# Kernel optimization log

Measured on AMD Instinct MI355X. Metric: run time of the kernel, lower is better.

The kernel has to match this reference:

```python
import jax, jax.numpy as jnp
import numpy as np

BETA = 0.25
B, D, H, W = 32, 256, 32, 32
K = 1024


def setup_inputs() -> dict:
    key = jax.random.key(0)
    k1, k2 = jax.random.split(key)
    inputs = jax.random.normal(k1, (B, D, H, W), dtype=jnp.float32)
    # torch init: uniform(-1/K, 1/K)
    codebook = jax.random.uniform(k2, (K, D), dtype=jnp.float32,
                                  minval=-1.0 / K, maxval=1.0 / K)
    return {"inputs": inputs, "codebook": codebook}


def reference(inputs, codebook):
    b, d, h, w = inputs.shape
    # (B, C, H, W) -> (B*H*W, D)
    x = inputs.transpose(0, 2, 3, 1).reshape(b * h * w, d)
    # Squared Euclidean distances; argmin is identical to cdist argmin.
    x2 = jnp.sum(x * x, axis=1, keepdims=True)            # (N, 1)
    c2 = jnp.sum(codebook * codebook, axis=1)             # (K,)
    d2 = x2 - 2.0 * (x @ codebook.T) + c2[None, :]        # (N, K)
    idx = jnp.argmin(d2, axis=1)                          # (N,)
    q = codebook[idx].reshape(b, h, w, d).transpose(0, 3, 1, 2)  # (B, D, H, W)

    q_loss = jnp.mean((q - jax.lax.stop_gradient(inputs)) ** 2)
    e_loss = jnp.mean((jax.lax.stop_gradient(q) - inputs) ** 2)
    vq_loss = q_loss + BETA * e_loss

    # straight-through estimator
    quantized = inputs + jax.lax.stop_gradient(q - inputs)
    return quantized, q_loss, e_loss, vq_loss, idx.reshape(b, h, w)
```

## Files before the change

kernel.cpp:

```cpp
#include <hip/hip_runtime.h>
#include <cstdint>

typedef float floatx4 __attribute__((ext_vector_type(4)));
typedef _Float16 half8 __attribute__((ext_vector_type(8)));
typedef _Float16 half4v __attribute__((ext_vector_type(4)));

#define D_DIM 256
#define HW 1024
#define K_CODES 1024
#define NPIX 32768
#define NELEM 8388608

#define OFF_QLOSS 8388608
#define OFF_ELOSS 8388609
#define OFF_VQ    8388610
#define OFF_IDX   8388611

#define WS_IDX     0
#define WS_C2      131072
#define WS_CNT     135168
#define WS_PART    135232
#define WS_FLAGPX  143424
#define WS_FLAGTOP 176192
#define WS_CBS     438336
#define FLAG_CAP   8192

#define MARGIN 2.5e-4f

__device__ __forceinline__ float np_pairwise_sq_256(const float* __restrict__ a, int stride) {
    float half[2];
#pragma unroll
    for (int h = 0; h < 2; ++h) {
        const float* p = a + (size_t)(h * 128) * stride;
        float r[8];
#pragma unroll
        for (int j = 0; j < 8; ++j) { float t = p[(size_t)j * stride]; r[j] = __fmul_rn(t, t); }
        for (int i = 8; i < 128; i += 8)
#pragma unroll
            for (int j = 0; j < 8; ++j) {
                float t = p[(size_t)(i + j) * stride];
                r[j] = __fadd_rn(r[j], __fmul_rn(t, t));
            }
        half[h] = __fadd_rn(__fadd_rn(__fadd_rn(r[0], r[1]), __fadd_rn(r[2], r[3])),
                            __fadd_rn(__fadd_rn(r[4], r[5]), __fadd_rn(r[6], r[7])));
    }
    return __fadd_rn(half[0], half[1]);
}

__global__ __launch_bounds__(256) void prep_kernel(const float* __restrict__ cb,
                                                   _Float16* __restrict__ cbs,
                                                   float* __restrict__ c2,
                                                   int* __restrict__ cnt) {
    int b = blockIdx.x;
    if (b < 256) {
        int idx = b * 256 + threadIdx.x;
        int c = idx >> 6;
        int d = (idx & 63) * 4;
        int s = d >> 5, q = (d >> 3) & 3, j0 = d & 7;
        int half = c >> 9, ch = (c >> 4) & 31, l15 = c & 15;
        int lane = q * 16 + l15;
        size_t o = ((((size_t)(half * 32 + ch) * 8 + s) * 64 + lane) * 8 + j0);
        floatx4 v = *(const floatx4*)(cb + (size_t)c * D_DIM + d);
        half4v h;
#pragma unroll
        for (int j = 0; j < 4; ++j) h[j] = (_Float16)(v[j] * 1024.0f);
        *(half4v*)(cbs + o) = h;
    } else {
        if (b == 256 && threadIdx.x == 0) *cnt = 0;
        int k = (b - 256) * 256 + threadIdx.x;
        c2[k] = np_pairwise_sq_256(cb + (size_t)k * D_DIM, 1);
    }
}

__device__ __forceinline__ void ins4v(float v, int k, float* S, int* I) {
    if (v < S[3]) {
        S[3] = v; I[3] = k;
#pragma unroll
        for (int j = 3; j > 0; --j) {
            if (S[j] < S[j - 1]) {
                float ts = S[j]; S[j] = S[j - 1]; S[j - 1] = ts;
                int   ti = I[j]; I[j] = I[j - 1]; I[j - 1] = ti;
            }
        }
    }
}

__global__ __launch_bounds__(256, 2) void gemm_swz(
        const float* __restrict__ x, const _Float16* __restrict__ cbs,
        const float* __restrict__ c2, float* __restrict__ out_idx,
        int* __restrict__ idxbuf, int* __restrict__ cnt,
        int* __restrict__ flagPx, floatx4* __restrict__ flagTop) {
    __shared__ float scr[4][32 * 33];

    const int t = threadIdx.x;
    const int w = t >> 6;
    const int l = t & 63;
    const int l15 = l & 15;
    const int q = l >> 4;
    const int pxg = w >> 1;
    const int half = w & 1;
    const int px0 = blockIdx.x * 32;
    const int bimg = px0 >> 10;
    const int hwb = (px0 & 1023) + pxg * 16;
    const float* xb = x + (size_t)bimg * (D_DIM * HW);

    half8 A[8];
    {
        float tmp[64];
#pragma unroll
        for (int s = 0; s < 8; ++s)
#pragma unroll
            for (int j = 0; j < 8; ++j)
                tmp[s * 8 + j] = xb[(size_t)(s * 32 + q * 8 + j) * HW + hwb + l15];
#pragma unroll
        for (int s = 0; s < 8; ++s) {
            half8 h;
#pragma unroll
            for (int j = 0; j < 8; ++j) h[j] = (_Float16)tmp[s * 8 + j];
            A[s] = h;
        }
    }

    const _Float16* base = cbs + (size_t)half * 131072;
    half8 B[2][8];
#pragma unroll
    for (int s = 0; s < 8; ++s)
        B[0][s] = *(const half8*)(base + (size_t)s * 512 + l * 8);
    float c2cur = c2[half * 512 + l15];

    float m1[4], m2[4]; int i1[4], i2[4];
#pragma unroll
    for (int a = 0; a < 4; ++a) {
        m1[a] = INFINITY; m2[a] = INFINITY; i1[a] = 0; i2[a] = 0;
    }

#pragma unroll 4
    for (int ch = 0; ch < 32; ++ch) {
        const int cur = ch & 1, nxt = cur ^ 1;
        float c2n = 0.f;
        if (ch < 31) {
            const _Float16* nb = base + (size_t)(ch + 1) * 4096;
#pragma unroll
            for (int s = 0; s < 8; ++s)
                B[nxt][s] = *(const half8*)(nb + (size_t)s * 512 + l * 8);
            c2n = c2[half * 512 + (ch + 1) * 16 + l15];
        }
        floatx4 ac[2];
        ac[0] = floatx4{0.f, 0.f, 0.f, 0.f};
        ac[1] = floatx4{0.f, 0.f, 0.f, 0.f};
#pragma unroll
        for (int s = 0; s < 4; ++s) {
            ac[0] = __builtin_amdgcn_mfma_f32_16x16x32_f16(A[s],     B[cur][s],     ac[0], 0, 0, 0);
            ac[1] = __builtin_amdgcn_mfma_f32_16x16x32_f16(A[s + 4], B[cur][s + 4], ac[1], 0, 0, 0);
        }
        const int code = half * 512 + ch * 16 + l15;
#pragma unroll
        for (int a = 0; a < 4; ++a) {
            float dot = ac[0][a] + ac[1][a];
            float s = fmaf(-0.001953125f, dot, c2cur);
            if (s < m1[a]) { m2[a] = m1[a]; i2[a] = i1[a]; m1[a] = s; i1[a] = code; }
            else if (s < m2[a]) { m2[a] = s; i2[a] = code; }
        }
        c2cur = c2n;
    }

    const int part = half * 16 + l15;
#pragma unroll
    for (int a = 0; a < 4; ++a) {
        int px = pxg * 16 + q * 4 + a;
        int o = part * 33 + px;
        scr[0][o] = m1[a];
        scr[1][o] = __int_as_float(i1[a]);
        scr[2][o] = m2[a];
        scr[3][o] = __int_as_float(i2[a]);
    }
    __syncthreads();
    if (t < 32) {
        float S[4] = {INFINITY, INFINITY, INFINITY, INFINITY};
        int   I[4] = {0x7fffffff, 0x7fffffff, 0x7fffffff, 0x7fffffff};
        for (int p = 0; p < 32; ++p) {
            int o = p * 33 + t;
            ins4v(scr[0][o], __float_as_int(scr[1][o]), S, I);
            ins4v(scr[2][o], __float_as_int(scr[3][o]), S, I);
        }
        int P = px0 + t;
        idxbuf[P] = I[0];
        out_idx[P] = (float)I[0];
        if (S[1] - S[0] <= MARGIN) {
            int pos = atomicAdd(cnt, 1);
            if (pos < FLAG_CAP) {
                flagPx[pos] = P;
                flagTop[2 * pos]     = floatx4{S[0], (float)I[0], S[1], (float)I[1]};
                flagTop[2 * pos + 1] = floatx4{S[2], (float)I[2], S[3], (float)I[3]};
            }
        }
    }
}

__global__ __launch_bounds__(256) void rescore_wave(
        const float* __restrict__ x, const float* __restrict__ cb,
        const float* __restrict__ c2, const int* __restrict__ cnt,
        const int* __restrict__ flagPx, const floatx4* __restrict__ flagTop,
        float* __restrict__ out_idx, int* __restrict__ idxbuf) {
    const int wglobal = blockIdx.x * 4 + (threadIdx.x >> 6);
    const int l = threadIdx.x & 63;
    int n = *cnt; if (n > FLAG_CAP) n = FLAG_CAP;
    for (int i = wglobal; i < n; i += 1024) {
        int P = flagPx[i];
        floatx4 ta = flagTop[2 * i], tb = flagTop[2 * i + 1];
        float s1 = ta[0];
        float cs[4] = {ta[0], ta[2], tb[0], tb[2]};
        int   ck[4] = {(int)ta[1], (int)ta[3], (int)tb[1], (int)tb[3]};
        int nc = 1;
        while (nc < 4 && cs[nc] - s1 <= MARGIN) ++nc;

        const float* xcol = x + (size_t)(P >> 10) * D_DIM * HW + (P & 1023);

        float rj = 0.f;
        if (l < 16) {
            int h = l >> 3, j = l & 7;
            const float* p = xcol + (size_t)(h * 128) * HW;
            float v0 = p[(size_t)j * HW];
            rj = __fmul_rn(v0, v0);
            for (int ii = 1; ii < 16; ++ii) {
                float v = p[(size_t)(ii * 8 + j) * HW];
                rj = __fadd_rn(rj, __fmul_rn(v, v));
            }
        }
        float r0 = __shfl(rj, 0), r1 = __shfl(rj, 1), r2 = __shfl(rj, 2), r3 = __shfl(rj, 3);
        float r4 = __shfl(rj, 4), r5 = __shfl(rj, 5), r6 = __shfl(rj, 6), r7 = __shfl(rj, 7);
        float h0 = __fadd_rn(__fadd_rn(__fadd_rn(r0, r1), __fadd_rn(r2, r3)),
                             __fadd_rn(__fadd_rn(r4, r5), __fadd_rn(r6, r7)));
        r0 = __shfl(rj, 8); r1 = __shfl(rj, 9); r2 = __shfl(rj, 10); r3 = __shfl(rj, 11);
        r4 = __shfl(rj, 12); r5 = __shfl(rj, 13); r6 = __shfl(rj, 14); r7 = __shfl(rj, 15);
        float h1 = __fadd_rn(__fadd_rn(__fadd_rn(r0, r1), __fadd_rn(r2, r3)),
                             __fadd_rn(__fadd_rn(r4, r5), __fadd_rn(r6, r7)));
        float x2 = __fadd_rn(h0, h1);

        float xv[4];
#pragma unroll
        for (int u = 0; u < 4; ++u) xv[u] = xcol[(size_t)(l + u * 64) * HW];
        double accd[4] = {0.0, 0.0, 0.0, 0.0};
        for (int jc = 0; jc < nc; ++jc) {
            const float* cr = cb + (size_t)ck[jc] * D_DIM;
            double a = 0.0;
#pragma unroll
            for (int u = 0; u < 4; ++u) a += (double)xv[u] * (double)cr[l + u * 64];
#pragma unroll
            for (int off = 32; off > 0; off >>= 1) a += __shfl_down(a, off);
            accd[jc] = a;
        }
        if (l == 0) {
            float bd = INFINITY; int bi = 0x7fffffff;
            for (int jc = 0; jc < nc; ++jc) {
                float mm = (float)accd[jc];
                float t1 = __fsub_rn(x2, __fmul_rn(2.0f, mm));
                float Dq = __fadd_rn(t1, c2[ck[jc]]);
                if (Dq < bd || (Dq == bd && ck[jc] < bi)) { bd = Dq; bi = ck[jc]; }
            }
            idxbuf[P] = bi;
            out_idx[P] = (float)bi;
        }
    }
}

__global__ __launch_bounds__(256) void quantize_loss_kernel(
        const float* __restrict__ x, const float* __restrict__ cb,
        const int* __restrict__ idxbuf, float* __restrict__ out_q,
        double* __restrict__ partials) {
    const int t = threadIdx.x;
    const int pxl = t & 31;
    const int dg = t >> 5;
    const int P = blockIdx.x * 32 + pxl;
    const int bimg = P >> 10, hw = P & 1023;
    const float* xb = x + (size_t)bimg * D_DIM * HW + hw;
    float* qb = out_q + (size_t)bimg * D_DIM * HW + hw;
    const floatx4* crow = (const floatx4*)(cb + (size_t)idxbuf[P] * D_DIM) + dg * 8;
    float lsum = 0.f;
#pragma unroll
    for (int i = 0; i < 8; ++i) {
        floatx4 cv = crow[i];
        int dbase = dg * 32 + i * 4;
#pragma unroll
        for (int j = 0; j < 4; ++j) {
            size_t off = (size_t)(dbase + j) * HW;
            float xv = xb[off];
            qb[off] = cv[j];
            float df = cv[j] - xv;
            lsum = fmaf(df, df, lsum);
        }
    }
    double ds = (double)lsum;
#pragma unroll
    for (int off = 32; off > 0; off >>= 1) ds += __shfl_down(ds, off);
    __shared__ double sred[4];
    if ((t & 63) == 0) sred[t >> 6] = ds;
    __syncthreads();
    if (t == 0) partials[blockIdx.x] = sred[0] + sred[1] + sred[2] + sred[3];
}

__global__ __launch_bounds__(64) void finalize_loss(const double* __restrict__ partials,
                                                    float* __restrict__ out) {
    double s = 0.0;
    for (int i = threadIdx.x; i < 1024; i += 64) s += partials[i];
#pragma unroll
    for (int off = 32; off > 0; off >>= 1) s += __shfl_down(s, off);
    if (threadIdx.x == 0) {
        double m = s / (double)NELEM;
        out[OFF_QLOSS] = (float)m;
        out[OFF_ELOSS] = (float)m;
        out[OFF_VQ]    = (float)(1.25 * m);
    }
}

extern "C" void kernel_launch(void* const* d_in, const int* in_sizes, int n_in,
                              void* d_out, int out_size, void* d_ws, size_t ws_size,
                              hipStream_t stream) {
    const float* x  = (const float*)d_in[0];
    const float* cb = (const float*)d_in[1];
    float* out = (float*)d_out;
    char* ws = (char*)d_ws;

    int*      idxbuf  = (int*)(ws + WS_IDX);
    float*    c2      = (float*)(ws + WS_C2);
    int*      cnt     = (int*)(ws + WS_CNT);
    double*   partials= (double*)(ws + WS_PART);
    int*      flagPx  = (int*)(ws + WS_FLAGPX);
    floatx4*  flagTop = (floatx4*)(ws + WS_FLAGTOP);
    _Float16* cbs     = (_Float16*)(ws + WS_CBS);

    prep_kernel<<<260, 256, 0, stream>>>(cb, cbs, c2, cnt);
    gemm_swz<<<NPIX / 32, 256, 0, stream>>>(x, cbs, c2, out + OFF_IDX, idxbuf,
                                            cnt, flagPx, flagTop);
    rescore_wave<<<256, 256, 0, stream>>>(x, cb, c2, cnt, flagPx, flagTop,
                                          out + OFF_IDX, idxbuf);
    quantize_loss_kernel<<<NPIX / 32, 256, 0, stream>>>(x, cb, idxbuf, out, partials);
    finalize_loss<<<1, 64, 0, stream>>>(partials, out);
}
```

Before: 166.4 us.

## Fuse rescore, quantize and loss finalization into one tail kernel

Merges the rescore, quantize/loss and finalize kernels into a single tail kernel, cutting two kernel launches and their dependency gaps. The GEMM pass now packs each flagged pixel's slot position into its index word, so every tail block rescores its own flagged pixels locally in shared memory. The final loss reduction is done by the last block to finish, detected with an atomic counter. In exchange, rescore work is spread unevenly across blocks, and the design depends on correct acquire/release ordering in the last-block pattern.

```diff
diff --git a/kernel.cpp b/kernel.cpp
--- a/kernel.cpp
+++ b/kernel.cpp
@@ -66,7 +66,7 @@
         for (int j = 0; j < 4; ++j) h[j] = (_Float16)(v[j] * 1024.0f);
         *(half4v*)(cbs + o) = h;
     } else {
-        if (b == 256 && threadIdx.x == 0) *cnt = 0;
+        if (b == 256 && threadIdx.x == 0) { cnt[0] = 0; cnt[1] = 0; }
         int k = (b - 256) * 256 + threadIdx.x;
         c2[k] = np_pairwise_sq_256(cb + (size_t)k * D_DIM, 1);
     }
@@ -87,9 +87,9 @@
 
 __global__ __launch_bounds__(256, 2) void gemm_swz(
         const float* __restrict__ x, const _Float16* __restrict__ cbs,
-        const float* __restrict__ c2, float* __restrict__ out_idx,
+        const float* __restrict__ c2,
         int* __restrict__ idxbuf, int* __restrict__ cnt,
-        int* __restrict__ flagPx, floatx4* __restrict__ flagTop) {
+        floatx4* __restrict__ flagTop) {
     __shared__ float scr[4][32 * 33];
 
     const int t = threadIdx.x;
@@ -184,30 +184,54 @@
             ins4v(scr[2][o], __float_as_int(scr[3][o]), S, I);
         }
         int P = px0 + t;
-        idxbuf[P] = I[0];
-        out_idx[P] = (float)I[0];
+        int rec = I[0];
         if (S[1] - S[0] <= MARGIN) {
             int pos = atomicAdd(cnt, 1);
             if (pos < FLAG_CAP) {
-                flagPx[pos] = P;
+                rec |= (pos + 1) << 10;
                 flagTop[2 * pos]     = floatx4{S[0], (float)I[0], S[1], (float)I[1]};
                 flagTop[2 * pos + 1] = floatx4{S[2], (float)I[2], S[3], (float)I[3]};
             }
         }
-    }
-}
-
-__global__ __launch_bounds__(256) void rescore_wave(
+        idxbuf[P] = rec;
+    }
+}
+
+__global__ __launch_bounds__(256) void tail_kernel(
         const float* __restrict__ x, const float* __restrict__ cb,
-        const float* __restrict__ c2, const int* __restrict__ cnt,
-        const int* __restrict__ flagPx, const floatx4* __restrict__ flagTop,
-        float* __restrict__ out_idx, int* __restrict__ idxbuf) {
-    const int wglobal = blockIdx.x * 4 + (threadIdx.x >> 6);
-    const int l = threadIdx.x & 63;
-    int n = *cnt; if (n > FLAG_CAP) n = FLAG_CAP;
-    for (int i = wglobal; i < n; i += 1024) {
-        int P = flagPx[i];
-        floatx4 ta = flagTop[2 * i], tb = flagTop[2 * i + 1];
+        const float* __restrict__ c2, const int* __restrict__ idxbuf,
+        const floatx4* __restrict__ flagTop, float* __restrict__ out,
+        double* __restrict__ partials, int* __restrict__ cd) {
+    __shared__ int finIdx[32];
+    __shared__ int flgPx[32];
+    __shared__ int flgPos[32];
+    __shared__ int nflag;
+    __shared__ int lastFlag;
+    __shared__ double sred[4];
+
+    const int t = threadIdx.x;
+    const int px0 = blockIdx.x * 32;
+
+    if (t == 0) nflag = 0;
+    __syncthreads();
+    if (t < 32) {
+        int v = idxbuf[px0 + t];
+        finIdx[t] = v & 1023;
+        int pos1 = v >> 10;
+        if (pos1 > 0) {
+            int m = atomicAdd(&nflag, 1);
+            flgPx[m] = t; flgPos[m] = pos1 - 1;
+        }
+    }
+    __syncthreads();
+
+    const int wv = t >> 6, l = t & 63;
+    const int nf = nflag;
+    for (int m = wv; m < nf; m += 4) {
+        const int pxl_ = flgPx[m];
+        const int pos  = flgPos[m];
+        const int P = px0 + pxl_;
+        floatx4 ta = flagTop[2 * pos], tb = flagTop[2 * pos + 1];
         float s1 = ta[0];
         float cs[4] = {ta[0], ta[2], tb[0], tb[2]};
         int   ck[4] = {(int)ta[1], (int)ta[3], (int)tb[1], (int)tb[3]};
@@ -258,24 +282,20 @@
                 float Dq = __fadd_rn(t1, c2[ck[jc]]);
                 if (Dq < bd || (Dq == bd && ck[jc] < bi)) { bd = Dq; bi = ck[jc]; }
             }
-            idxbuf[P] = bi;
-            out_idx[P] = (float)bi;
-        }
-    }
-}
-
-__global__ __launch_bounds__(256) void quantize_loss_kernel(
-        const float* __restrict__ x, const float* __restrict__ cb,
-        const int* __restrict__ idxbuf, float* __restrict__ out_q,
-        double* __restrict__ partials) {
-    const int t = threadIdx.x;
+            finIdx[pxl_] = bi;
+        }
+    }
+    __syncthreads();
+
+    if (t < 32) out[OFF_IDX + px0 + t] = (float)finIdx[t];
+
     const int pxl = t & 31;
     const int dg = t >> 5;
-    const int P = blockIdx.x * 32 + pxl;
+    const int P = px0 + pxl;
     const int bimg = P >> 10, hw = P & 1023;
     const float* xb = x + (size_t)bimg * D_DIM * HW + hw;
-    float* qb = out_q + (size_t)bimg * D_DIM * HW + hw;
-    const floatx4* crow = (const floatx4*)(cb + (size_t)idxbuf[P] * D_DIM) + dg * 8;
+    float* qb = out + (size_t)bimg * D_DIM * HW + hw;
+    const floatx4* crow = (const floatx4*)(cb + (size_t)finIdx[pxl] * D_DIM) + dg * 8;
     float lsum = 0.f;
 #pragma unroll
     for (int i = 0; i < 8; ++i) {
@@ -293,23 +313,32 @@
     double ds = (double)lsum;
 #pragma unroll
     for (int off = 32; off > 0; off >>= 1) ds += __shfl_down(ds, off);
-    __shared__ double sred[4];
     if ((t & 63) == 0) sred[t >> 6] = ds;
     __syncthreads();
-    if (t == 0) partials[blockIdx.x] = sred[0] + sred[1] + sred[2] + sred[3];
-}
-
-__global__ __launch_bounds__(64) void finalize_loss(const double* __restrict__ partials,
-                                                    float* __restrict__ out) {
-    double s = 0.0;
-    for (int i = threadIdx.x; i < 1024; i += 64) s += partials[i];
-#pragma unroll
-    for (int off = 32; off > 0; off >>= 1) s += __shfl_down(s, off);
-    if (threadIdx.x == 0) {
-        double m = s / (double)NELEM;
-        out[OFF_QLOSS] = (float)m;
-        out[OFF_ELOSS] = (float)m;
-        out[OFF_VQ]    = (float)(1.25 * m);
+
+    if (t == 0) {
+        double tot = sred[0] + sred[1] + sred[2] + sred[3];
+        __hip_atomic_store(&partials[blockIdx.x], tot,
+                           __ATOMIC_RELAXED, __HIP_MEMORY_SCOPE_AGENT);
+        int prev = __hip_atomic_fetch_add(&cd[1], 1,
+                                          __ATOMIC_ACQ_REL, __HIP_MEMORY_SCOPE_AGENT);
+        lastFlag = (prev == 1023);
+    }
+    __syncthreads();
+    if (lastFlag) {
+        double s = 0.0;
+        for (int i = t; i < 1024; i += 256)
+            s += __hip_atomic_load(&partials[i], __ATOMIC_RELAXED, __HIP_MEMORY_SCOPE_AGENT);
+#pragma unroll
+        for (int off = 32; off > 0; off >>= 1) s += __shfl_down(s, off);
+        if ((t & 63) == 0) sred[t >> 6] = s;
+        __syncthreads();
+        if (t == 0) {
+            double m = (sred[0] + sred[1] + sred[2] + sred[3]) / (double)NELEM;
+            out[OFF_QLOSS] = (float)m;
+            out[OFF_ELOSS] = (float)m;
+            out[OFF_VQ]    = (float)(1.25 * m);
+        }
     }
 }
 
@@ -323,17 +352,13 @@
 
     int*      idxbuf  = (int*)(ws + WS_IDX);
     float*    c2      = (float*)(ws + WS_C2);
-    int*      cnt     = (int*)(ws + WS_CNT);
+    int*      cd      = (int*)(ws + WS_CNT);
     double*   partials= (double*)(ws + WS_PART);
-    int*      flagPx  = (int*)(ws + WS_FLAGPX);
     floatx4*  flagTop = (floatx4*)(ws + WS_FLAGTOP);
     _Float16* cbs     = (_Float16*)(ws + WS_CBS);
 
-    prep_kernel<<<260, 256, 0, stream>>>(cb, cbs, c2, cnt);
-    gemm_swz<<<NPIX / 32, 256, 0, stream>>>(x, cbs, c2, out + OFF_IDX, idxbuf,
-                                            cnt, flagPx, flagTop);
-    rescore_wave<<<256, 256, 0, stream>>>(x, cb, c2, cnt, flagPx, flagTop,
-                                          out + OFF_IDX, idxbuf);
-    quantize_loss_kernel<<<NPIX / 32, 256, 0, stream>>>(x, cb, idxbuf, out, partials);
-    finalize_loss<<<1, 64, 0, stream>>>(partials, out);
-}
+    prep_kernel<<<260, 256, 0, stream>>>(cb, cbs, c2, cd);
+    gemm_swz<<<NPIX / 32, 256, 0, stream>>>(x, cbs, c2, idxbuf, cd, flagTop);
+    tail_kernel<<<NPIX / 32, 256, 0, stream>>>(x, cb, c2, idxbuf, flagTop,
+                                               out, partials, cd);
+}
```

Measured after the change: 197.5 us. +18.7%, slower.

## Restructure quantize pass for coalesced rows and fuse loss finalize via last-block atomic

Applied to the files above, without the earlier changes.

The quantize/loss kernel now assigns each block one channel across four images, so x loads and output stores are contiguous float4 rows instead of strided per-pixel accesses. The codebook is gathered per element through the index buffer. The separate finalize kernel is removed: each block publishes its partial sum, and the last block to increment an atomic counter reduces all partials and writes the losses. This saves one launch and improves coalescing, at the cost of scattered codebook gathers and reusing the flagTop workspace region for partials.

```diff
diff --git a/kernel.cpp b/kernel.cpp
--- a/kernel.cpp
+++ b/kernel.cpp
@@ -66,7 +66,7 @@
         for (int j = 0; j < 4; ++j) h[j] = (_Float16)(v[j] * 1024.0f);
         *(half4v*)(cbs + o) = h;
     } else {
-        if (b == 256 && threadIdx.x == 0) *cnt = 0;
+        if (b == 256 && threadIdx.x == 0) { cnt[0] = 0; cnt[1] = 0; }
         int k = (b - 256) * 256 + threadIdx.x;
         c2[k] = np_pairwise_sq_256(cb + (size_t)k * D_DIM, 1);
     }
@@ -264,52 +264,64 @@
     }
 }
 
-__global__ __launch_bounds__(256) void quantize_loss_kernel(
+__global__ __launch_bounds__(256) void quant_stream(
         const float* __restrict__ x, const float* __restrict__ cb,
-        const int* __restrict__ idxbuf, float* __restrict__ out_q,
-        double* __restrict__ partials) {
+        const int* __restrict__ idxbuf, float* __restrict__ out,
+        double* __restrict__ partials, int* __restrict__ cd) {
+    __shared__ double sred[4];
+    __shared__ int lastFlag;
     const int t = threadIdx.x;
-    const int pxl = t & 31;
-    const int dg = t >> 5;
-    const int P = blockIdx.x * 32 + pxl;
-    const int bimg = P >> 10, hw = P & 1023;
-    const float* xb = x + (size_t)bimg * D_DIM * HW + hw;
-    float* qb = out_q + (size_t)bimg * D_DIM * HW + hw;
-    const floatx4* crow = (const floatx4*)(cb + (size_t)idxbuf[P] * D_DIM) + dg * 8;
+    const int d = blockIdx.x >> 3;
+    const int img0 = (blockIdx.x & 7) * 4;
+
     float lsum = 0.f;
 #pragma unroll
-    for (int i = 0; i < 8; ++i) {
-        floatx4 cv = crow[i];
-        int dbase = dg * 32 + i * 4;
-#pragma unroll
-        for (int j = 0; j < 4; ++j) {
-            size_t off = (size_t)(dbase + j) * HW;
-            float xv = xb[off];
-            qb[off] = cv[j];
-            float df = cv[j] - xv;
+    for (int i = 0; i < 4; ++i) {
+        const int img = img0 + i;
+        const size_t rowo = ((size_t)img * D_DIM + d) * HW + t * 4;
+        floatx4 xv = *(const floatx4*)(x + rowo);
+        int4 iv = *(const int4*)(idxbuf + img * HW + t * 4);
+        floatx4 cv;
+        cv[0] = cb[(size_t)iv.x * D_DIM + d];
+        cv[1] = cb[(size_t)iv.y * D_DIM + d];
+        cv[2] = cb[(size_t)iv.z * D_DIM + d];
+        cv[3] = cb[(size_t)iv.w * D_DIM + d];
+        *(floatx4*)(out + rowo) = cv;
+#pragma unroll
+        for (int k = 0; k < 4; ++k) {
+            float df = cv[k] - xv[k];
             lsum = fmaf(df, df, lsum);
         }
     }
     double ds = (double)lsum;
 #pragma unroll
     for (int off = 32; off > 0; off >>= 1) ds += __shfl_down(ds, off);
-    __shared__ double sred[4];
     if ((t & 63) == 0) sred[t >> 6] = ds;
     __syncthreads();
-    if (t == 0) partials[blockIdx.x] = sred[0] + sred[1] + sred[2] + sred[3];
-}
-
-__global__ __launch_bounds__(64) void finalize_loss(const double* __restrict__ partials,
-                                                    float* __restrict__ out) {
-    double s = 0.0;
-    for (int i = threadIdx.x; i < 1024; i += 64) s += partials[i];
-#pragma unroll
-    for (int off = 32; off > 0; off >>= 1) s += __shfl_down(s, off);
-    if (threadIdx.x == 0) {
-        double m = s / (double)NELEM;
-        out[OFF_QLOSS] = (float)m;
-        out[OFF_ELOSS] = (float)m;
-        out[OFF_VQ]    = (float)(1.25 * m);
+
+    if (t == 0) {
+        double tot = sred[0] + sred[1] + sred[2] + sred[3];
+        __hip_atomic_store(&partials[blockIdx.x], tot,
+                           __ATOMIC_RELAXED, __HIP_MEMORY_SCOPE_AGENT);
+        int prev = __hip_atomic_fetch_add(&cd[1], 1,
+                                          __ATOMIC_ACQ_REL, __HIP_MEMORY_SCOPE_AGENT);
+        lastFlag = (prev == 2047);
+    }
+    __syncthreads();
+    if (lastFlag) {
+        double s = 0.0;
+        for (int i = t; i < 2048; i += 256)
+            s += __hip_atomic_load(&partials[i], __ATOMIC_RELAXED, __HIP_MEMORY_SCOPE_AGENT);
+#pragma unroll
+        for (int off = 32; off > 0; off >>= 1) s += __shfl_down(s, off);
+        if ((t & 63) == 0) sred[t >> 6] = s;
+        __syncthreads();
+        if (t == 0) {
+            double m = (sred[0] + sred[1] + sred[2] + sred[3]) / (double)NELEM;
+            out[OFF_QLOSS] = (float)m;
+            out[OFF_ELOSS] = (float)m;
+            out[OFF_VQ]    = (float)(1.25 * m);
+        }
     }
 }
 
@@ -323,17 +335,16 @@
 
     int*      idxbuf  = (int*)(ws + WS_IDX);
     float*    c2      = (float*)(ws + WS_C2);
-    int*      cnt     = (int*)(ws + WS_CNT);
-    double*   partials= (double*)(ws + WS_PART);
+    int*      cd      = (int*)(ws + WS_CNT);
     int*      flagPx  = (int*)(ws + WS_FLAGPX);
     floatx4*  flagTop = (floatx4*)(ws + WS_FLAGTOP);
+    double*   partials= (double*)(ws + WS_FLAGTOP);
     _Float16* cbs     = (_Float16*)(ws + WS_CBS);
 
-    prep_kernel<<<260, 256, 0, stream>>>(cb, cbs, c2, cnt);
+    prep_kernel<<<260, 256, 0, stream>>>(cb, cbs, c2, cd);
     gemm_swz<<<NPIX / 32, 256, 0, stream>>>(x, cbs, c2, out + OFF_IDX, idxbuf,
-                                            cnt, flagPx, flagTop);
-    rescore_wave<<<256, 256, 0, stream>>>(x, cb, c2, cnt, flagPx, flagTop,
+                                            cd, flagPx, flagTop);
+    rescore_wave<<<256, 256, 0, stream>>>(x, cb, c2, cd, flagPx, flagTop,
                                           out + OFF_IDX, idxbuf);
-    quantize_loss_kernel<<<NPIX / 32, 256, 0, stream>>>(x, cb, idxbuf, out, partials);
-    finalize_loss<<<1, 64, 0, stream>>>(partials, out);
-}
+    quant_stream<<<2048, 256, 0, stream>>>(x, cb, idxbuf, out, partials, cd);
+}
```

Result: slower. 246.0 us (+47.9%).
